# Performance work log

Hardware: AMD Instinct MI355X
Metric: run time of the kernel (lower is better)

The kernel has to match this reference:

```python
import jax, jax.numpy as jnp
import numpy as np

N_NODES = 100000
N_EDGES = 1600000
DIM = 128
BN_EPS = 1e-5


def setup_inputs() -> dict:
    key = jax.random.key(0)
    k1, k2, k3, k4 = jax.random.split(key, 4)
    scale = 1.0 / np.sqrt(DIM)
    return {
        "x": jax.random.normal(k1, (N_NODES, DIM), dtype=jnp.float32),
        "edge_index": jax.random.randint(k2, (2, N_EDGES), 0, N_NODES, dtype=jnp.int64),
        "W_l": jax.random.normal(k3, (DIM, DIM), dtype=jnp.float32) * scale,
        "b_l": jnp.zeros((DIM,), dtype=jnp.float32),
        "W_r": jax.random.normal(k4, (DIM, DIM), dtype=jnp.float32) * scale,
        "gamma": jnp.ones((DIM,), dtype=jnp.float32),
        "beta": jnp.zeros((DIM,), dtype=jnp.float32),
    }


def reference(x, edge_index, W_l, b_l, W_r, gamma, beta):
    n = x.shape[0]
    src, dst = edge_index[0], edge_index[1]
    # SAGEConv mean aggregation: gather source features, scatter-sum to dst, divide by degree
    agg = jax.ops.segment_sum(x[src], dst, num_segments=n)          # [N, d_in]
    deg = jax.ops.segment_sum(jnp.ones_like(src, dtype=x.dtype), dst, num_segments=n)
    mean = agg / jnp.maximum(deg, 1.0)[:, None]
    # lin_l(mean) + lin_r(x)  (bias lives in lin_l, PyG default)
    h = mean @ W_l + b_l + x @ W_r                                   # [N, d_out]
    # act -> BatchNorm1d (training mode, batch stats) -> dropout(p=0, identity)
    h = jax.nn.relu(h)
    mu = jnp.mean(h, axis=0)
    var = jnp.mean(jnp.square(h - mu), axis=0)                       # biased var, as torch BN
    h = (h - mu) * jax.lax.rsqrt(var + BN_EPS) * gamma + beta
    # residual
    return x + h
```

## Files before the change

### kernel.cpp

```cpp
#include <hip/hip_runtime.h>

#define DIM 128
#define BN_EPS 1e-5f
#define NB 32
#define NBK_MAX 512

typedef __attribute__((ext_vector_type(8))) short bf16x8;
typedef __attribute__((ext_vector_type(4))) float f32x4;

union B8 { uint4 u; bf16x8 s; };

__device__ __forceinline__ ushort f2bf(float f) {
    unsigned u = __float_as_uint(f);
    u += 0x7fffu + ((u >> 16) & 1u);
    return (ushort)(u >> 16);
}

__global__ void k_prep(const float4* __restrict__ x4, const float* __restrict__ Wl,
                       const float* __restrict__ Wr, const unsigned* __restrict__ eiu,
                       int* __restrict__ bcnt, uint2* __restrict__ xf8,
                       uint4* __restrict__ xbf, uint4* __restrict__ wpack,
                       int nn, int ne, int PB, int WB) {
    __shared__ int nz;
    __shared__ int lh[NBK_MAX];
    int b = blockIdx.x;
    const int tid = threadIdx.x;

    if (b < PB) {
        const int t = b * 256 + tid;
        const int n8 = nn * DIM / 8;
        if (t < n8) {
            const float4 a = x4[2 * t], c = x4[2 * t + 1];
            int u0 = __builtin_amdgcn_cvt_pk_fp8_f32(a.x, a.y, 0, false);
            u0 = __builtin_amdgcn_cvt_pk_fp8_f32(a.z, a.w, u0, true);
            int u1 = __builtin_amdgcn_cvt_pk_fp8_f32(c.x, c.y, 0, false);
            u1 = __builtin_amdgcn_cvt_pk_fp8_f32(c.z, c.w, u1, true);
            xf8[t] = make_uint2((unsigned)u0, (unsigned)u1);
            uint4 xb;
            xb.x = ((unsigned)f2bf(a.y) << 16) | f2bf(a.x);
            xb.y = ((unsigned)f2bf(a.w) << 16) | f2bf(a.z);
            xb.z = ((unsigned)f2bf(c.y) << 16) | f2bf(c.x);
            xb.w = ((unsigned)f2bf(c.w) << 16) | f2bf(c.z);
            xbf[t] = xb;
        }
        return;
    }
    b -= PB;
    if (b < WB) {
        const int t = b * 256 + tid;
        const int lane = t & 63, kk = (t >> 6) & 3, nt = (t >> 8) & 7, mat = t >> 11;
        const float* W = mat ? Wr : Wl;
        const int k0 = kk * 32 + (lane >> 4) * 8;
        const int n = nt * 16 + (lane & 15);
        ushort e[8];
#pragma unroll
        for (int j = 0; j < 8; ++j) e[j] = f2bf(W[(size_t)(k0 + j) * DIM + n]);
        uint4 o;
        o.x = ((unsigned)e[1] << 16) | e[0];
        o.y = ((unsigned)e[3] << 16) | e[2];
        o.z = ((unsigned)e[5] << 16) | e[4];
        o.w = ((unsigned)e[7] << 16) | e[6];
        wpack[t] = o;
        return;
    }
    b -= WB;
    const int nbk = (nn + 255) >> 8;
    for (int i = tid; i < nbk; i += 256) lh[i] = 0;
    if (tid == 0) nz = 0;
    __syncthreads();
    const int e0 = b * 4096;
    {
        int es = e0 + tid * 16;
        if (es >= ne) es = ne - 1;
        if (eiu[2 * (size_t)es + 1] != 0) atomicOr(&nz, 1);
    }
    __syncthreads();
    const int is64 = (nz == 0);
    for (int j = 0; j < 16; ++j) {
        const int e = e0 + j * 256 + tid;
        if (e < ne) {
            int dst;
            if (is64) dst = (int)((const long long*)eiu)[(size_t)ne + e];
            else      dst = ((const int*)eiu)[(size_t)ne + e];
            atomicAdd(&lh[dst >> 8], 1);
        }
    }
    __syncthreads();
    for (int i = tid; i < nbk; i += 256)
        if (lh[i]) atomicAdd(&bcnt[i], lh[i]);
}

__global__ __launch_bounds__(512) void k_scanb(const int* __restrict__ bcnt,
                                               int* __restrict__ bbase,
                                               int* __restrict__ cursor2, int nn, int ne) {
    __shared__ int sd[512];
    const int nbk = (nn + 255) >> 8;
    const int tid = threadIdx.x;
    const int v = (tid < nbk) ? bcnt[tid] : 0;
    sd[tid] = v;
    __syncthreads();
    for (int ofs = 1; ofs < 512; ofs <<= 1) {
        const int t = (tid >= ofs) ? sd[tid - ofs] : 0;
        __syncthreads();
        sd[tid] += t;
        __syncthreads();
    }
    if (tid < nbk) {
        const int ex = sd[tid] - v;
        bbase[tid] = ex;
        cursor2[tid] = ex;
    }
    if (tid == 0) bbase[nbk] = ne;
}

__global__ __launch_bounds__(256) void k_passA(const unsigned* __restrict__ eiu,
                                               int* __restrict__ cursor2,
                                               unsigned* __restrict__ pairbuf,
                                               int nn, int ne) {
    __shared__ int lh[NBK_MAX];
    __shared__ int gb[NBK_MAX];
    __shared__ int nz;
    const int nbk = (nn + 255) >> 8;
    const int tid = threadIdx.x;
    const int e0 = blockIdx.x * 4096;
    for (int i = tid; i < nbk; i += 256) lh[i] = 0;
    if (tid == 0) nz = 0;
    __syncthreads();
    {
        int es = e0 + tid * 16;
        if (es >= ne) es = ne - 1;
        if (eiu[2 * (size_t)es + 1] != 0) atomicOr(&nz, 1);
    }
    __syncthreads();
    const int is64 = (nz == 0);
    unsigned pay[16];
    int bkrank[16];
#pragma unroll
    for (int j = 0; j < 16; ++j) {
        const int e = e0 + j * 256 + tid;
        bkrank[j] = -1;
        if (e < ne) {
            int src, dst;
            if (is64) {
                const long long* p = (const long long*)eiu;
                src = (int)p[e];
                dst = (int)p[(size_t)ne + e];
            } else {
                const int* p = (const int*)eiu;
                src = p[e];
                dst = p[(size_t)ne + e];
            }
            const int bk = dst >> 8;
            const int rank = atomicAdd(&lh[bk], 1);
            bkrank[j] = (bk << 16) | rank;
            pay[j] = ((unsigned)(dst & 255) << 24) | (unsigned)src;
        }
    }
    __syncthreads();
    for (int i = tid; i < nbk; i += 256) {
        const int c = lh[i];
        gb[i] = c ? atomicAdd(&cursor2[i], c) : 0;
    }
    __syncthreads();
#pragma unroll
    for (int j = 0; j < 16; ++j) {
        if (bkrank[j] >= 0) {
            const int bk = bkrank[j] >> 16, rank = bkrank[j] & 0xFFFF;
            pairbuf[gb[bk] + rank] = pay[j];
        }
    }
}

__global__ __launch_bounds__(256) void k_passB(const unsigned* __restrict__ pairbuf,
                                               const int* __restrict__ bbase,
                                               int2* __restrict__ off2,
                                               int* __restrict__ srcbuf, int nn) {
    __shared__ int cl[256];
    __shared__ int sd[256];
    __shared__ int cur[256];
    const int tid = threadIdx.x;
    const int b = blockIdx.x;
    const int node0 = b << 8;
    const int e0 = bbase[b], e1 = bbase[b + 1];
    cl[tid] = 0;
    __syncthreads();
    for (int e = e0 + tid; e < e1; e += 256)
        atomicAdd(&cl[pairbuf[e] >> 24], 1);
    __syncthreads();
    const int v = cl[tid];
    sd[tid] = v;
    __syncthreads();
    for (int ofs = 1; ofs < 256; ofs <<= 1) {
        const int t = (tid >= ofs) ? sd[tid - ofs] : 0;
        __syncthreads();
        sd[tid] += t;
        __syncthreads();
    }
    const int ex = sd[tid] - v;
    cur[tid] = ex;
    const int node = node0 + tid;
    if (node < nn) off2[node] = make_int2(e0 + ex, v);
    __syncthreads();
    for (int e = e0 + tid; e < e1; e += 256) {
        const unsigned p = pairbuf[e];
        const int pos = atomicAdd(&cur[p >> 24], 1);
        srcbuf[e0 + pos] = (int)(p & 0xFFFFFFu);
    }
}

__global__ __launch_bounds__(512) void k_gemm(
    const uint4* __restrict__ xbf, const uint2* __restrict__ xf8,
    const uint4* __restrict__ wpack, const float* __restrict__ bl,
    const int2* __restrict__ off2, const int* __restrict__ srcbuf,
    ushort* __restrict__ hout, float* __restrict__ ssum, float* __restrict__ ssq,
    int nn)
{
    __shared__ uint4 mean4[NB * 16];
    __shared__ uint4 xls4[NB * 16];
    __shared__ float red_sum[2][DIM];
    __shared__ float red_sq[2][DIM];

    const int tid = threadIdx.x;
    const int lane = tid & 63;
    const int w = tid >> 6;
    const int base = blockIdx.x * NB;
    const int q = lane & 15;

#define CVT8(v)                                                           \
    {                                                                     \
        auto p0 = __builtin_amdgcn_cvt_pk_f32_fp8((v).x, false);          \
        auto p1 = __builtin_amdgcn_cvt_pk_f32_fp8((v).x, true);           \
        auto p2 = __builtin_amdgcn_cvt_pk_f32_fp8((v).y, false);          \
        auto p3 = __builtin_amdgcn_cvt_pk_f32_fp8((v).y, true);           \
        acc[0] += p0[0]; acc[1] += p0[1]; acc[2] += p1[0]; acc[3] += p1[1]; \
        acc[4] += p2[0]; acc[5] += p2[1]; acc[6] += p3[0]; acc[7] += p3[1]; \
    }

    {
        const int ln = w * 4 + (lane >> 4);
        const int node = base + ln;
        const int slot = q ^ (ln & 15);
        float acc[8];
#pragma unroll
        for (int j = 0; j < 8; ++j) acc[j] = 0.f;
        int o = 0, c = 0;

        if (node < nn) {
            xls4[ln * 16 + slot] = xbf[(size_t)node * 16 + q];
            const int2 oc = off2[node];
            o = oc.x;
            c = oc.y;
        } else {
            xls4[ln * 16 + slot] = make_uint4(0, 0, 0, 0);
        }

        const int* sp = srcbuf + o;
        int e = 0;
        if (c >= 8) {
            uint2 va[8];
            {
                int s[8];
#pragma unroll
                for (int j = 0; j < 8; ++j) s[j] = sp[j];
#pragma unroll
                for (int j = 0; j < 8; ++j) va[j] = xf8[(size_t)s[j] * 16 + q];
            }
            for (e = 8; e + 8 <= c; e += 8) {
                int sb[8];
#pragma unroll
                for (int j = 0; j < 8; ++j) sb[j] = sp[e + j];
                uint2 vb[8];
#pragma unroll
                for (int j = 0; j < 8; ++j) vb[j] = xf8[(size_t)sb[j] * 16 + q];
#pragma unroll
                for (int j = 0; j < 8; ++j) CVT8(va[j]);
#pragma unroll
                for (int j = 0; j < 8; ++j) va[j] = vb[j];
            }
#pragma unroll
            for (int j = 0; j < 8; ++j) CVT8(va[j]);
        }
        for (; e < c; ++e) {
            const uint2 v = xf8[(size_t)sp[e] * 16 + q];
            CVT8(v);
        }
        const float r = 1.0f / fmaxf((float)c, 1.0f);
#pragma unroll
        for (int j = 0; j < 8; ++j) acc[j] *= r;
#undef CVT8

        uint4 mp;
        mp.x = ((unsigned)f2bf(acc[1]) << 16) | f2bf(acc[0]);
        mp.y = ((unsigned)f2bf(acc[3]) << 16) | f2bf(acc[2]);
        mp.z = ((unsigned)f2bf(acc[5]) << 16) | f2bf(acc[4]);
        mp.w = ((unsigned)f2bf(acc[7]) << 16) | f2bf(acc[6]);
        mean4[ln * 16 + slot] = mp;
    }
    __syncthreads();

    const int m = w & 1;
    const int nh = w >> 1;
    const int row16 = lane & 15;
    const int kgrp = lane >> 4;
    const int ln2 = m * 16 + row16;

    bf16x8 am[4], ax[4];
#pragma unroll
    for (int kk = 0; kk < 4; ++kk) {
        const int unit = (kk * 4 + kgrp) ^ row16;
        B8 va, vb;
        va.u = mean4[ln2 * 16 + unit];
        vb.u = xls4[ln2 * 16 + unit];
        am[kk] = va.s;
        ax[kk] = vb.s;
    }

    f32x4 acc2[2];
#pragma unroll
    for (int j = 0; j < 2; ++j) {
        const float bv = bl[(nh * 2 + j) * 16 + row16];
        acc2[j] = (f32x4){bv, bv, bv, bv};
    }

#pragma unroll
    for (int j = 0; j < 2; ++j) {
        const int nt = nh * 2 + j;
        const uint4* pl = wpack + (size_t)(nt * 4) * 64 + lane;
        const uint4* pr = wpack + (size_t)((8 + nt) * 4) * 64 + lane;
        B8 wl[4], wr[4];
#pragma unroll
        for (int kk = 0; kk < 4; ++kk) {
            wl[kk].u = pl[kk * 64];
            wr[kk].u = pr[kk * 64];
        }
#pragma unroll
        for (int kk = 0; kk < 4; ++kk)
            acc2[j] = __builtin_amdgcn_mfma_f32_16x16x32_bf16(am[kk], wl[kk].s, acc2[j], 0, 0, 0);
#pragma unroll
        for (int kk = 0; kk < 4; ++kk)
            acc2[j] = __builtin_amdgcn_mfma_f32_16x16x32_bf16(ax[kk], wr[kk].s, acc2[j], 0, 0, 0);
    }

#pragma unroll
    for (int j = 0; j < 2; ++j) {
        const int feat = (nh * 2 + j) * 16 + row16;
        float s = 0.f, sq = 0.f;
#pragma unroll
        for (int r = 0; r < 4; ++r) {
            const int node = base + m * 16 + kgrp * 4 + r;
            const float v = fmaxf(acc2[j][r], 0.0f);
            if (node < nn) {
                hout[(size_t)node * DIM + feat] = f2bf(v);
                s += v;
                sq += v * v;
            }
        }
        s += __shfl_xor(s, 16);
        s += __shfl_xor(s, 32);
        sq += __shfl_xor(sq, 16);
        sq += __shfl_xor(sq, 32);
        if (lane < 16) {
            red_sum[m][feat] = s;
            red_sq[m][feat] = sq;
        }
    }
    __syncthreads();
    if (tid < DIM) {
        atomicAdd(&ssum[tid], red_sum[0][tid] + red_sum[1][tid]);
        atomicAdd(&ssq[tid], red_sq[0][tid] + red_sq[1][tid]);
    }
}

__global__ __launch_bounds__(512) void k_finalize(
    const uint4* __restrict__ xbf, const uint4* __restrict__ h4,
    const float* __restrict__ ssum, const float* __restrict__ ssq,
    const float* __restrict__ gamma, const float* __restrict__ beta,
    float4* __restrict__ out4, int nn)
{
    const float invN = 1.0f / (float)nn;
    const int tid = threadIdx.x;
    const int node = blockIdx.x * 32 + (tid >> 4);
    const int q = tid & 15;
    if (node >= nn) return;
    const uint4 hv = h4[(size_t)node * 16 + q];
    const uint4 xv = xbf[(size_t)node * 16 + q];
    const float4 s4a = ((const float4*)ssum)[2 * q], s4b = ((const float4*)ssum)[2 * q + 1];
    const float4 q4a = ((const float4*)ssq)[2 * q], q4b = ((const float4*)ssq)[2 * q + 1];
    const float4 g4a = ((const float4*)gamma)[2 * q], g4b = ((const float4*)gamma)[2 * q + 1];
    const float4 b4a = ((const float4*)beta)[2 * q], b4b = ((const float4*)beta)[2 * q + 1];
    float h[8], x[8];
    h[0] = __uint_as_float(hv.x << 16);
    h[1] = __uint_as_float(hv.x & 0xffff0000u);
    h[2] = __uint_as_float(hv.y << 16);
    h[3] = __uint_as_float(hv.y & 0xffff0000u);
    h[4] = __uint_as_float(hv.z << 16);
    h[5] = __uint_as_float(hv.z & 0xffff0000u);
    h[6] = __uint_as_float(hv.w << 16);
    h[7] = __uint_as_float(hv.w & 0xffff0000u);
    x[0] = __uint_as_float(xv.x << 16);
    x[1] = __uint_as_float(xv.x & 0xffff0000u);
    x[2] = __uint_as_float(xv.y << 16);
    x[3] = __uint_as_float(xv.y & 0xffff0000u);
    x[4] = __uint_as_float(xv.z << 16);
    x[5] = __uint_as_float(xv.z & 0xffff0000u);
    x[6] = __uint_as_float(xv.w << 16);
    x[7] = __uint_as_float(xv.w & 0xffff0000u);
    float4 oa, ob;
    {
        const float mu = s4a.x * invN, rs = rsqrtf(q4a.x * invN - mu * mu + BN_EPS);
        oa.x = x[0] + (h[0] - mu) * rs * g4a.x + b4a.x;
    }
    {
        const float mu = s4a.y * invN, rs = rsqrtf(q4a.y * invN - mu * mu + BN_EPS);
        oa.y = x[1] + (h[1] - mu) * rs * g4a.y + b4a.y;
    }
    {
        const float mu = s4a.z * invN, rs = rsqrtf(q4a.z * invN - mu * mu + BN_EPS);
        oa.z = x[2] + (h[2] - mu) * rs * g4a.z + b4a.z;
    }
    {
        const float mu = s4a.w * invN, rs = rsqrtf(q4a.w * invN - mu * mu + BN_EPS);
        oa.w = x[3] + (h[3] - mu) * rs * g4a.w + b4a.w;
    }
    {
        const float mu = s4b.x * invN, rs = rsqrtf(q4b.x * invN - mu * mu + BN_EPS);
        ob.x = x[4] + (h[4] - mu) * rs * g4b.x + b4b.x;
    }
    {
        const float mu = s4b.y * invN, rs = rsqrtf(q4b.y * invN - mu * mu + BN_EPS);
        ob.y = x[5] + (h[5] - mu) * rs * g4b.y + b4b.y;
    }
    {
        const float mu = s4b.z * invN, rs = rsqrtf(q4b.z * invN - mu * mu + BN_EPS);
        ob.z = x[6] + (h[6] - mu) * rs * g4b.z + b4b.z;
    }
    {
        const float mu = s4b.w * invN, rs = rsqrtf(q4b.w * invN - mu * mu + BN_EPS);
        ob.w = x[7] + (h[7] - mu) * rs * g4b.w + b4b.w;
    }
    out4[(size_t)node * 32 + 2 * q] = oa;
    out4[(size_t)node * 32 + 2 * q + 1] = ob;
}

extern "C" void kernel_launch(void* const* d_in, const int* in_sizes, int n_in,
                              void* d_out, int out_size, void* d_ws, size_t ws_size,
                              hipStream_t stream) {
    const float* x     = (const float*)d_in[0];
    const void*  ei    = d_in[1];
    const float* Wl    = (const float*)d_in[2];
    const float* bl    = (const float*)d_in[3];
    const float* Wr    = (const float*)d_in[4];
    const float* gamma = (const float*)d_in[5];
    const float* beta  = (const float*)d_in[6];
    float* out = (float*)d_out;

    const int nn = in_sizes[0] / DIM;
    const int ne = in_sizes[1] / 2;
    const int nbk = (nn + 255) >> 8;

    int* ws = (int*)d_ws;
    int*   bcnt    = ws;
    float* ssum    = (float*)(ws + 512);
    float* ssq     = (float*)(ws + 640);
    int*   bbase   = ws + 768;
    int*   cursor2 = ws + 1280;
    int2*  off2    = (int2*)(ws + 1792);
    size_t pos = 1792 + 2 * (size_t)nn;
    pos = (pos + 3) & ~(size_t)3;
    uint4* wpack  = (uint4*)(ws + pos);
    int*   srcbuf = (int*)(wpack + 4096);
    size_t p2 = (size_t)(srcbuf + ne - ws);
    p2 = (p2 + 3) & ~(size_t)3;
    uint2* xf8 = (uint2*)(ws + p2);
    unsigned* pairbuf = (unsigned*)(xf8 + (size_t)nn * 16);
    ushort*   hbuf    = (ushort*)pairbuf;
    uint4*    xbf     = (uint4*)(hbuf + (size_t)nn * DIM);

    hipMemsetAsync(d_ws, 0, 768 * sizeof(int), stream);

    const int PB = (nn * DIM / 8 + 255) / 256;
    const int WB = 16;
    const int HB = (ne + 4095) / 4096;
    k_prep<<<PB + WB + HB, 256, 0, stream>>>((const float4*)x, Wl, Wr,
                                             (const unsigned*)ei, bcnt, xf8, xbf, wpack,
                                             nn, ne, PB, WB);
    k_scanb<<<1, 512, 0, stream>>>(bcnt, bbase, cursor2, nn, ne);
    k_passA<<<(ne + 4095) / 4096, 256, 0, stream>>>((const unsigned*)ei, cursor2,
                                                    pairbuf, nn, ne);
    k_passB<<<nbk, 256, 0, stream>>>(pairbuf, bbase, off2, srcbuf, nn);
    const int ntile = (nn + NB - 1) / NB;
    k_gemm<<<ntile, 512, 0, stream>>>(xbf, xf8, wpack, bl,
                                      off2, srcbuf, hbuf, ssum, ssq, nn);
    k_finalize<<<(nn + 31) / 32, 512, 0, stream>>>(xbf, (const uint4*)hbuf,
                                                   ssum, ssq, gamma, beta,
                                                   (float4*)out, nn);
}
```

Baseline: 189.4 us.

## Simplify gather loop with padded batches, add occupancy hint, enlarge histogram blocks

Replaces the software-pipelined neighbor gather (double-buffered va/vb plus scalar tail loop) with a single batched loop of 8 clamped loads, zeroing out-of-range entries, to cut register pressure. Adds a min-blocks hint to the gemm kernel's launch bounds to raise occupancy. Separately, histogram blocks in the prep kernel now cover 16384 edges instead of 4096, reducing global atomic merges. The simplified gather gives up explicit prefetch overlap and does redundant loads for partial batches, and it relies on the zero-valued fp8 byte decoding to 0.

```diff
diff --git a/kernel.cpp b/kernel.cpp
--- a/kernel.cpp
+++ b/kernel.cpp
@@ -68,15 +68,15 @@
     for (int i = tid; i < nbk; i += 256) lh[i] = 0;
     if (tid == 0) nz = 0;
     __syncthreads();
-    const int e0 = b * 4096;
-    {
-        int es = e0 + tid * 16;
+    const int e0 = b * 16384;
+    {
+        int es = e0 + tid;
         if (es >= ne) es = ne - 1;
         if (eiu[2 * (size_t)es + 1] != 0) atomicOr(&nz, 1);
     }
     __syncthreads();
     const int is64 = (nz == 0);
-    for (int j = 0; j < 16; ++j) {
+    for (int j = 0; j < 64; ++j) {
         const int e = e0 + j * 256 + tid;
         if (e < ne) {
             int dst;
@@ -208,7 +208,7 @@
     }
 }
 
-__global__ __launch_bounds__(512) void k_gemm(
+__global__ __launch_bounds__(512, 4) void k_gemm(
     const uint4* __restrict__ xbf, const uint2* __restrict__ xf8,
     const uint4* __restrict__ wpack, const float* __restrict__ bl,
     const int2* __restrict__ off2, const int* __restrict__ srcbuf,
@@ -255,34 +255,21 @@
         }
 
         const int* sp = srcbuf + o;
-        int e = 0;
-        if (c >= 8) {
-            uint2 va[8];
-            {
-                int s[8];
-#pragma unroll
-                for (int j = 0; j < 8; ++j) s[j] = sp[j];
-#pragma unroll
-                for (int j = 0; j < 8; ++j) va[j] = xf8[(size_t)s[j] * 16 + q];
+        for (int e = 0; e < c; e += 8) {
+            int s[8];
+#pragma unroll
+            for (int j = 0; j < 8; ++j) {
+                const int idx = e + j;
+                s[j] = sp[(idx < c) ? idx : (c - 1)];
             }
-            for (e = 8; e + 8 <= c; e += 8) {
-                int sb[8];
-#pragma unroll
-                for (int j = 0; j < 8; ++j) sb[j] = sp[e + j];
-                uint2 vb[8];
-#pragma unroll
-                for (int j = 0; j < 8; ++j) vb[j] = xf8[(size_t)sb[j] * 16 + q];
-#pragma unroll
-                for (int j = 0; j < 8; ++j) CVT8(va[j]);
-#pragma unroll
-                for (int j = 0; j < 8; ++j) va[j] = vb[j];
+            uint2 v[8];
+#pragma unroll
+            for (int j = 0; j < 8; ++j) v[j] = xf8[(size_t)s[j] * 16 + q];
+#pragma unroll
+            for (int j = 0; j < 8; ++j) {
+                if (e + j >= c) { v[j].x = 0u; v[j].y = 0u; }
+                CVT8(v[j]);
             }
-#pragma unroll
-            for (int j = 0; j < 8; ++j) CVT8(va[j]);
-        }
-        for (; e < c; ++e) {
-            const uint2 v = xf8[(size_t)sp[e] * 16 + q];
-            CVT8(v);
         }
         const float r = 1.0f / fmaxf((float)c, 1.0f);
 #pragma unroll
@@ -480,7 +467,7 @@
 
     const int PB = (nn * DIM / 8 + 255) / 256;
     const int WB = 16;
-    const int HB = (ne + 4095) / 4096;
+    const int HB = (ne + 16383) / 16384;
     k_prep<<<PB + WB + HB, 256, 0, stream>>>((const float4*)x, Wl, Wr,
                                              (const unsigned*)ei, bcnt, xf8, xbf, wpack,
                                              nn, ne, PB, WB);
```

Measured after the change: 191.2 us. No clear change (+1.0%).
